# Performance work log

Measured on AMD Instinct MI355X. Metric: run time of the kernel, lower is better.

Reference implementation:

```python
import jax, jax.numpy as jnp
import numpy as np

N_ATOMS = 51200
N_MOL = 512
FEAT = 384


def setup_inputs() -> dict:
    key = jax.random.key(0)
    ks = jax.random.split(key, 20)
    s = 0.05  # small random weights instead of the degenerate zero-init
    inp = {
        "node_feats": jax.random.normal(ks[0], (N_ATOMS, FEAT), jnp.float32),
        "energy": jax.random.normal(ks[1], (N_MOL,), jnp.float32),
        "forces": jax.random.normal(ks[2], (N_ATOMS, 3), jnp.float32),
        "stress": jax.random.normal(ks[3], (N_MOL, 3, 3), jnp.float32),
        "W1": jax.random.normal(ks[4], (64, 256), jnp.float32) * s,
        "b1": jnp.zeros((64,), jnp.float32),
        "W2": jax.random.normal(ks[5], (16, 64), jnp.float32) * s,
        "b2": jnp.zeros((16,), jnp.float32),
        "W3": jax.random.normal(ks[6], (1, 16), jnp.float32) * s,
        "b3": jnp.zeros((1,), jnp.float32),
        "W1f": jax.random.normal(ks[7], (64, 256), jnp.float32) * s,
        "b1f": jnp.zeros((64,), jnp.float32),
        "W2f": jax.random.normal(ks[8], (16, 64), jnp.float32) * s,
        "b2f": jnp.zeros((16,), jnp.float32),
        "W3f": jax.random.normal(ks[9], (1, 16), jnp.float32) * s,
        "b3f": jnp.zeros((1,), jnp.float32),
        "S_uncert": jnp.zeros((1,), jnp.float32),
        # atom -> molecule segment ids (sorted, every molecule non-empty)
        "batch_idx": jnp.repeat(jnp.arange(N_MOL, dtype=jnp.int64), N_ATOMS // N_MOL),
    }
    return inp


def _mlp(x, W1, b1, W2, b2, W3, b3):
    h = jax.nn.silu(x @ W1.T + b1)
    h = jax.nn.silu(h @ W2.T + b2)
    return h @ W3.T + b3  # [N, 1]


def reference(node_feats, energy, forces, stress,
              W1, b1, W2, b2, W3, b3,
              W1f, b1f, W2f, b2f, W3f, b3f,
              S_uncert, batch_idx):
    # concat first 128 and last 128 feature channels -> [N, 256]
    nf = jnp.concatenate([node_feats[:, :128], node_feats[:, -128:]], axis=1)

    # E head: faithfully zeroed out and replaced by constant 0.6
    e_stds = jnp.exp(_mlp(nf, W1, b1, W2, b2, W3, b3))[:, 0] * 0 + 0.6  # [N]
    # F head
    f_u = jnp.exp(_mlp(nf, W1f, b1f, W2f, b2f, W3f, b3f))[:, 0] * 0.1   # [N]
    force_uncert = jnp.stack([f_u, f_u, f_u], axis=-1)                  # [N, 3]
    # stress uncert: constant 0.1/16 (S_uncert term zeroed, kept faithfully)
    stress_uncert = jnp.ones_like(stress) * jnp.exp(S_uncert[0]) * 0 + 0.1 / 16

    # per-molecule mean of e_stds via segment sums (scatter_add in torch)
    eu_sum = jax.ops.segment_sum(e_stds, batch_idx, num_segments=N_MOL)
    n_atoms = jax.ops.segment_sum(jnp.ones_like(e_stds), batch_idx, num_segments=N_MOL)
    energy_uncert = eu_sum / n_atoms  # [n_mol]

    return (energy, forces, stress, energy_uncert, force_uncert, stress_uncert)
```

## Files before the change

kernel.cpp:

```cpp
#include <hip/hip_runtime.h>
#include <hip/hip_bf16.h>

#define N_ATOMS 51200

#define OUT_FUNC 159232

typedef __attribute__((ext_vector_type(4))) float f32x4;
typedef __attribute__((ext_vector_type(4))) short s16x4;
typedef __attribute__((ext_vector_type(8))) short s16x8;

constexpr int BLK = 256;

__device__ __forceinline__ short f2bf(float x) {
    union { __hip_bfloat16 b; short s; } u;
    u.b = __float2bfloat16(x);
    return u.s;
}
__device__ __forceinline__ float silu_(float v) { return v / (1.0f + __expf(-v)); }
__device__ __forceinline__ s16x8 cvt8(f32x4 lo, f32x4 hi) {
    s16x8 f;
    f[0]=f2bf(lo.x); f[1]=f2bf(lo.y); f[2]=f2bf(lo.z); f[3]=f2bf(lo.w);
    f[4]=f2bf(hi.x); f[5]=f2bf(hi.y); f[6]=f2bf(hi.z); f[7]=f2bf(hi.w);
    return f;
}

__global__ __launch_bounds__(BLK, 5) void funcert_kernel(
    const float* __restrict__ nf,
    const float* __restrict__ energy,
    const float* __restrict__ forces,
    const float* __restrict__ stress,
    const float* __restrict__ W1f, const float* __restrict__ b1f,
    const float* __restrict__ W2f, const float* __restrict__ b2f,
    const float* __restrict__ W3f, const float* __restrict__ b3f,
    float* __restrict__ out)
{
    const int t   = threadIdx.x;
    const int gid = blockIdx.x * BLK + t;

    if (gid < 40960) {
        f32x4 v; int o = gid;
        if      (gid < 128)   { v = ((const f32x4*)energy)[gid]; }
        else if (gid < 38528) { v = ((const f32x4*)forces)[gid - 128]; }
        else if (gid < 39680) { v = ((const f32x4*)stress)[gid - 38528]; }
        else if (gid < 39808) { v = (f32x4){0.6f, 0.6f, 0.6f, 0.6f}; }
        else { v = (f32x4){0.00625f, 0.00625f, 0.00625f, 0.00625f}; o = gid + 38400; }
        ((f32x4*)out)[o] = v;
    }

    __shared__ short Xs[64 * 128];
    __shared__ short H1s[64 * 64];

    const int lane  = t & 63;
    const int w     = t >> 6;
    const int g     = lane >> 4;
    const int col   = lane & 15;
    const int abase = blockIdx.x * 64;

    const int ch  = w * 16 + col;
    const float b1v = b1f[ch];

    const int c4  = lane & 31;
    const int sub = lane >> 5;

    f32x4 acc[4];
    #pragma unroll
    for (int mt = 0; mt < 4; ++mt) acc[mt] = (f32x4){0.f, 0.f, 0.f, 0.f};

    #pragma unroll 1
    for (int h = 0; h < 2; ++h) {
        #pragma unroll
        for (int i = 0; i < 8; ++i) {
            const int r = i * 8 + w * 2 + sub;
            const f32x4 x = ((const f32x4*)nf)[(size_t)(abase + r) * 96 + h * 64 + c4];
            const int sp = (c4 >> 1) ^ (r & 7);
            s16x4 bb;
            bb.x = f2bf(x.x); bb.y = f2bf(x.y); bb.z = f2bf(x.z); bb.w = f2bf(x.w);
            *(s16x4*)(Xs + r * 128 + sp * 8 + (lane & 1) * 4) = bb;
        }

        f32x4 wv[8];
        #pragma unroll
        for (int ks = 0; ks < 4; ++ks) {
            const float* p = W1f + ch * 256 + h * 128 + ks * 32 + g * 8;
            wv[2 * ks]     = *(const f32x4*)p;
            wv[2 * ks + 1] = *(const f32x4*)(p + 4);
        }
        __syncthreads();

        s16x8 wf[4];
        #pragma unroll
        for (int ks = 0; ks < 4; ++ks) wf[ks] = cvt8(wv[2 * ks], wv[2 * ks + 1]);

        #pragma unroll
        for (int mt = 0; mt < 4; ++mt) {
            const int row = mt * 16 + col;
            #pragma unroll
            for (int ks = 0; ks < 4; ++ks) {
                const int sl = (ks * 4 + g) ^ (row & 7);
                const s16x8 af = *(const s16x8*)(Xs + row * 128 + sl * 8);
                acc[mt] = __builtin_amdgcn_mfma_f32_16x16x32_bf16(af, wf[ks], acc[mt], 0, 0, 0);
            }
        }
        if (h == 0) __syncthreads();
    }

    #pragma unroll
    for (int mt = 0; mt < 4; ++mt) {
        #pragma unroll
        for (int r = 0; r < 4; ++r) {
            const int atom = mt * 16 + g * 4 + r;
            H1s[atom * 64 + ch] = f2bf(silu_(acc[mt][r] + b1v));
        }
    }
    __syncthreads();

    s16x8 w2frag[2];
    #pragma unroll
    for (int ks = 0; ks < 2; ++ks) {
        const float* p = W2f + col * 64 + ks * 32 + g * 8;
        w2frag[ks] = cvt8(*(const f32x4*)p, *(const f32x4*)(p + 4));
    }
    const int arow = w * 16 + col;
    f32x4 a2 = {0.f, 0.f, 0.f, 0.f};
    #pragma unroll
    for (int ks = 0; ks < 2; ++ks) {
        const s16x8 af = *(const s16x8*)(H1s + arow * 64 + ks * 32 + g * 8);
        a2 = __builtin_amdgcn_mfma_f32_16x16x32_bf16(af, w2frag[ks], a2, 0, 0, 0);
    }

    const float b2v = b2f[col];
    const float w3v = W3f[col];
    float y[4];
    #pragma unroll
    for (int r = 0; r < 4; ++r)
        y[r] = silu_(a2[r] + b2v) * w3v;
    #pragma unroll
    for (int m = 1; m < 16; m <<= 1) {
        #pragma unroll
        for (int r = 0; r < 4; ++r)
            y[r] += __shfl_xor(y[r], m, 64);
    }
    const float b3v = b3f[0];
    float fu[4];
    #pragma unroll
    for (int r = 0; r < 4; ++r)
        fu[r] = __expf(y[r] + b3v) * 0.1f;

    if (col < 12) {
        const int a_ = col / 3, c = col - a_ * 3;
        const float v = (a_ == 0) ? fu[0] : (a_ == 1) ? fu[1] : (a_ == 2) ? fu[2] : fu[3];
        const int atom = w * 16 + g * 4 + a_;
        out[OUT_FUNC + 3 * (abase + atom) + c] = v;
    }
}

extern "C" void kernel_launch(void* const* d_in, const int* in_sizes, int n_in,
                              void* d_out, int out_size, void* d_ws, size_t ws_size,
                              hipStream_t stream) {
    const float* nf     = (const float*)d_in[0];
    const float* energy = (const float*)d_in[1];
    const float* forces = (const float*)d_in[2];
    const float* stress = (const float*)d_in[3];
    const float* W1f    = (const float*)d_in[10];
    const float* b1f    = (const float*)d_in[11];
    const float* W2f    = (const float*)d_in[12];
    const float* b2f    = (const float*)d_in[13];
    const float* W3f    = (const float*)d_in[14];
    const float* b3f    = (const float*)d_in[15];
    float* out = (float*)d_out;

    dim3 grid(N_ATOMS / 64);
    funcert_kernel<<<grid, BLK, 0, stream>>>(nf, energy, forces, stress,
                                             W1f, b1f, W2f, b2f, W3f, b3f, out);
}
```

Measured before the change: 22.79 us.

## Pipeline node-feature loads in quarter chunks with double-buffered LDS and truncating bf16 packs

Splits the 256-wide K dimension into four 64-wide quarters. Global loads for later quarters are issued into registers before the MFMA work on earlier quarters, with two LDS buffers alternating. The feature loads are also moved ahead of the passthrough copy so more memory traffic is in flight. The bf16 conversion switches from round-to-nearest to truncation via byte permute, which costs fewer instructions but changes numerics slightly. Launch bounds drop to 4 waves per SIMD to allow the extra prefetch registers.

```diff
diff --git a/kernel.cpp b/kernel.cpp
--- a/kernel.cpp
+++ b/kernel.cpp
@@ -6,25 +6,27 @@
 #define OUT_FUNC 159232
 
 typedef __attribute__((ext_vector_type(4))) float f32x4;
-typedef __attribute__((ext_vector_type(4))) short s16x4;
+typedef __attribute__((ext_vector_type(2))) unsigned u32x2;
+typedef __attribute__((ext_vector_type(4))) unsigned u32x4;
 typedef __attribute__((ext_vector_type(8))) short s16x8;
 
 constexpr int BLK = 256;
 
-__device__ __forceinline__ short f2bf(float x) {
-    union { __hip_bfloat16 b; short s; } u;
-    u.b = __float2bfloat16(x);
-    return u.s;
+__device__ __forceinline__ unsigned pack2(float lo, float hi) {
+    return __builtin_amdgcn_perm(__float_as_uint(hi), __float_as_uint(lo), 0x07060302);
+}
+__device__ __forceinline__ s16x8 pack8(f32x4 lo, f32x4 hi) {
+    union { u32x4 u; s16x8 s; } c;
+    c.u.x = pack2(lo.x, lo.y); c.u.y = pack2(lo.z, lo.w);
+    c.u.z = pack2(hi.x, hi.y); c.u.w = pack2(hi.z, hi.w);
+    return c.s;
+}
+__device__ __forceinline__ short bftrunc(float x) {
+    return (short)(__float_as_uint(x) >> 16);
 }
 __device__ __forceinline__ float silu_(float v) { return v / (1.0f + __expf(-v)); }
-__device__ __forceinline__ s16x8 cvt8(f32x4 lo, f32x4 hi) {
-    s16x8 f;
-    f[0]=f2bf(lo.x); f[1]=f2bf(lo.y); f[2]=f2bf(lo.z); f[3]=f2bf(lo.w);
-    f[4]=f2bf(hi.x); f[5]=f2bf(hi.y); f[6]=f2bf(hi.z); f[7]=f2bf(hi.w);
-    return f;
-}
-
-__global__ __launch_bounds__(BLK, 5) void funcert_kernel(
+
+__global__ __launch_bounds__(BLK, 4) void funcert_kernel(
     const float* __restrict__ nf,
     const float* __restrict__ energy,
     const float* __restrict__ forces,
@@ -37,6 +39,66 @@
     const int t   = threadIdx.x;
     const int gid = blockIdx.x * BLK + t;
 
+    __shared__ short Xq[2][64 * 64];
+    __shared__ short H1s[64 * 64];
+
+    const int lane  = t & 63;
+    const int w     = t >> 6;
+    const int g     = lane >> 4;
+    const int col   = lane & 15;
+    const int abase = blockIdx.x * 64;
+    const int ch    = w * 16 + col;
+
+    const int rb  = t >> 4;
+    const int f4c = t & 15;
+    const float4* nfr = (const float4*)nf + (size_t)(abase + rb) * 96 + f4c;
+    const int wbyte0 = rb * 128 + (f4c & 1) * 8;
+
+    #define XQ_ISSUE(dst, qb)                                            \
+        { _Pragma("unroll")                                              \
+          for (int i = 0; i < 4; ++i)                                    \
+              dst[i] = *(const f32x4*)(nfr + (size_t)i * 16 * 96 + (qb)); }
+
+    #define XQ_STASH(buf, src)                                           \
+        { _Pragma("unroll")                                              \
+          for (int i = 0; i < 4; ++i) {                                  \
+              const int r = rb + 16 * i;                                 \
+              u32x2 bb;                                                  \
+              bb.x = pack2(src[i].x, src[i].y);                          \
+              bb.y = pack2(src[i].z, src[i].w);                          \
+              *(u32x2*)((char*)(buf) + (wbyte0 + 2048 * i +              \
+                        ((((f4c >> 1) ^ (r & 7))) << 4))) = bb;          \
+          } }
+
+    #define WQ_ISSUE(dst, q)                                             \
+        { _Pragma("unroll")                                              \
+          for (int ks2 = 0; ks2 < 2; ++ks2) {                            \
+              const float* p = W1f + ch * 256 + (q) * 64 + ks2 * 32 + g * 8; \
+              dst[2 * ks2]     = *(const f32x4*)p;                       \
+              dst[2 * ks2 + 1] = *(const f32x4*)(p + 4);                 \
+          } }
+
+    #define Q_COMPUTE(buf, wf)                                           \
+        { _Pragma("unroll")                                              \
+          for (int mt = 0; mt < 4; ++mt) {                               \
+              const int row = mt * 16 + col;                             \
+              _Pragma("unroll")                                          \
+              for (int ks2 = 0; ks2 < 2; ++ks2) {                        \
+                  const int sl = (ks2 * 4 + g) ^ (row & 7);              \
+                  const s16x8 af = *(const s16x8*)((buf) + row * 64 + sl * 8); \
+                  acc[mt] = __builtin_amdgcn_mfma_f32_16x16x32_bf16(af, wf[ks2], acc[mt], 0, 0, 0); \
+              } } }
+
+    f32x4 xa[4], xb[4], wv[4];
+    s16x8 wf[2];
+    f32x4 acc[4];
+    #pragma unroll
+    for (int mt = 0; mt < 4; ++mt) acc[mt] = (f32x4){0.f, 0.f, 0.f, 0.f};
+
+    XQ_ISSUE(xa, 0);
+    XQ_ISSUE(xb, 16);
+    WQ_ISSUE(wv, 0);
+
     if (gid < 40960) {
         f32x4 v; int o = gid;
         if      (gid < 128)   { v = ((const f32x4*)energy)[gid]; }
@@ -46,70 +108,42 @@
         else { v = (f32x4){0.00625f, 0.00625f, 0.00625f, 0.00625f}; o = gid + 38400; }
         ((f32x4*)out)[o] = v;
     }
-
-    __shared__ short Xs[64 * 128];
-    __shared__ short H1s[64 * 64];
-
-    const int lane  = t & 63;
-    const int w     = t >> 6;
-    const int g     = lane >> 4;
-    const int col   = lane & 15;
-    const int abase = blockIdx.x * 64;
-
-    const int ch  = w * 16 + col;
     const float b1v = b1f[ch];
 
-    const int c4  = lane & 31;
-    const int sub = lane >> 5;
-
-    f32x4 acc[4];
-    #pragma unroll
-    for (int mt = 0; mt < 4; ++mt) acc[mt] = (f32x4){0.f, 0.f, 0.f, 0.f};
-
-    #pragma unroll 1
-    for (int h = 0; h < 2; ++h) {
-        #pragma unroll
-        for (int i = 0; i < 8; ++i) {
-            const int r = i * 8 + w * 2 + sub;
-            const f32x4 x = ((const f32x4*)nf)[(size_t)(abase + r) * 96 + h * 64 + c4];
-            const int sp = (c4 >> 1) ^ (r & 7);
-            s16x4 bb;
-            bb.x = f2bf(x.x); bb.y = f2bf(x.y); bb.z = f2bf(x.z); bb.w = f2bf(x.w);
-            *(s16x4*)(Xs + r * 128 + sp * 8 + (lane & 1) * 4) = bb;
-        }
-
-        f32x4 wv[8];
-        #pragma unroll
-        for (int ks = 0; ks < 4; ++ks) {
-            const float* p = W1f + ch * 256 + h * 128 + ks * 32 + g * 8;
-            wv[2 * ks]     = *(const f32x4*)p;
-            wv[2 * ks + 1] = *(const f32x4*)(p + 4);
-        }
-        __syncthreads();
-
-        s16x8 wf[4];
-        #pragma unroll
-        for (int ks = 0; ks < 4; ++ks) wf[ks] = cvt8(wv[2 * ks], wv[2 * ks + 1]);
-
-        #pragma unroll
-        for (int mt = 0; mt < 4; ++mt) {
-            const int row = mt * 16 + col;
-            #pragma unroll
-            for (int ks = 0; ks < 4; ++ks) {
-                const int sl = (ks * 4 + g) ^ (row & 7);
-                const s16x8 af = *(const s16x8*)(Xs + row * 128 + sl * 8);
-                acc[mt] = __builtin_amdgcn_mfma_f32_16x16x32_bf16(af, wf[ks], acc[mt], 0, 0, 0);
-            }
-        }
-        if (h == 0) __syncthreads();
-    }
+    wf[0] = pack8(wv[0], wv[1]); wf[1] = pack8(wv[2], wv[3]);
+    XQ_STASH(Xq[0], xa);
+    __syncthreads();
+    XQ_ISSUE(xa, 64);
+    WQ_ISSUE(wv, 1);
+    Q_COMPUTE(Xq[0], wf);
+    __syncthreads();
+
+    wf[0] = pack8(wv[0], wv[1]); wf[1] = pack8(wv[2], wv[3]);
+    XQ_STASH(Xq[1], xb);
+    __syncthreads();
+    XQ_ISSUE(xb, 80);
+    WQ_ISSUE(wv, 2);
+    Q_COMPUTE(Xq[1], wf);
+    __syncthreads();
+
+    wf[0] = pack8(wv[0], wv[1]); wf[1] = pack8(wv[2], wv[3]);
+    XQ_STASH(Xq[0], xa);
+    __syncthreads();
+    WQ_ISSUE(wv, 3);
+    Q_COMPUTE(Xq[0], wf);
+    __syncthreads();
+
+    wf[0] = pack8(wv[0], wv[1]); wf[1] = pack8(wv[2], wv[3]);
+    XQ_STASH(Xq[1], xb);
+    __syncthreads();
+    Q_COMPUTE(Xq[1], wf);
 
     #pragma unroll
     for (int mt = 0; mt < 4; ++mt) {
         #pragma unroll
         for (int r = 0; r < 4; ++r) {
             const int atom = mt * 16 + g * 4 + r;
-            H1s[atom * 64 + ch] = f2bf(silu_(acc[mt][r] + b1v));
+            H1s[atom * 64 + ch] = bftrunc(silu_(acc[mt][r] + b1v));
         }
     }
     __syncthreads();
@@ -118,7 +152,7 @@
     #pragma unroll
     for (int ks = 0; ks < 2; ++ks) {
         const float* p = W2f + col * 64 + ks * 32 + g * 8;
-        w2frag[ks] = cvt8(*(const f32x4*)p, *(const f32x4*)(p + 4));
+        w2frag[ks] = pack8(*(const f32x4*)p, *(const f32x4*)(p + 4));
     }
     const int arow = w * 16 + col;
     f32x4 a2 = {0.f, 0.f, 0.f, 0.f};
```

Result: faster. 20.89 us (-8.3%).
